# Kernel tuning notes

Hardware: AMD Instinct MI355X
Metric: run time of the kernel (lower is better)

## Reference

```python
import jax, jax.numpy as jnp
import numpy as np

B, S, D, H = 2, 2048, 1024, 16
HD = D // H
SCALING = HD ** -0.5


def _length_mask(lengths, seqlen):
    return (jnp.arange(seqlen)[None, :] < jnp.asarray(lengths)[:, None]).astype(jnp.int32)


def setup_inputs() -> dict:
    key = jax.random.key(0)
    ks = jax.random.split(key, 10)
    std = D ** -0.5
    inp = {
        "hidden_states": jax.random.normal(ks[0], (B, S, D), dtype=jnp.float32),
        "Wq": jax.random.normal(ks[1], (D, D), dtype=jnp.float32) * std,
        "bq": jax.random.normal(ks[2], (D,), dtype=jnp.float32) * 0.02,
        "Wk": jax.random.normal(ks[3], (D, D), dtype=jnp.float32) * std,
        "bk": jax.random.normal(ks[4], (D,), dtype=jnp.float32) * 0.02,
        "Wv": jax.random.normal(ks[5], (D, D), dtype=jnp.float32) * std,
        "bv": jax.random.normal(ks[6], (D,), dtype=jnp.float32) * 0.02,
        "Wo": jax.random.normal(ks[7], (D, D), dtype=jnp.float32) * std,
        "bo": jax.random.normal(ks[8], (D,), dtype=jnp.float32) * 0.02,
        # variable valid lengths per batch element (padding at the end)
        "query_mask_1d": _length_mask([S, S - 512], S),
        "key_mask_1d": _length_mask([S, S - 512], S),
    }
    return inp


def reference(hidden_states, Wq, bq, Wk, bk, Wv, bv, Wo, bo, query_mask_1d, key_mask_1d):
    bsz, tgt_len, _ = hidden_states.shape
    # projections (dropout p=0 / eval -> identity)
    q = (hidden_states @ Wq + bq) * SCALING
    k = hidden_states @ Wk + bk
    v = hidden_states @ Wv + bv
    q = q.reshape(bsz, tgt_len, H, HD).transpose(0, 2, 1, 3)  # [B,H,S,HD]
    k = k.reshape(bsz, -1, H, HD).transpose(0, 2, 1, 3)
    v = v.reshape(bsz, -1, H, HD).transpose(0, 2, 1, 3)

    scores = jnp.einsum("bhqd,bhkd->bhqk", q, k)  # [B,H,S,S]
    q_valid = (query_mask_1d != 0)[:, None, :, None]  # [B,1,S,1]
    k_valid = (key_mask_1d != 0)[:, None, None, :]    # [B,1,1,S]
    # masked_fill(-inf) on padded keys; padded-query rows would be all -inf ->
    # softmax NaN -> nan_to_num(0). We compute the same result NaN-free by
    # zeroing the scores of padded-query rows and zeroing their probs after.
    s = jnp.where(k_valid, scores, -jnp.inf)
    s = jnp.where(q_valid, s, 0.0)
    attn_weights = jax.nn.softmax(s, axis=-1) * q_valid  # == softmax + nan_to_num

    attn_output = jnp.einsum("bhqk,bhkd->bhqd", attn_weights, v)
    attn_output = attn_output.transpose(0, 2, 1, 3).reshape(bsz, tgt_len, D)
    attn_output = attn_output @ Wo + bo
    return attn_output
```

## Files before the change

### kernel.cpp

```cpp
#include <hip/hip_runtime.h>
#include <stdint.h>

#define BB 2
#define SS 2048
#define DD 1024
#define HH 16
#define HDIM 64
#define MTOT (BB*SS)
#define QK_SCALE_LOG2E 0.180336880f

typedef unsigned short u16;
typedef __attribute__((ext_vector_type(8))) __bf16 bf16x8;
typedef __attribute__((ext_vector_type(4))) float f32x4;

static __device__ __forceinline__ float exp2_hw(float x) {
    return __builtin_amdgcn_exp2f(x);
}

static __device__ __forceinline__ u16 f2bu(float f) {
    union { float f; uint32_t u; } c; c.f = f;
    uint32_t u = c.u + 0x7fffu + ((c.u >> 16) & 1u);
    return (u16)(u >> 16);
}

static __device__ __forceinline__ u16 f2b_hw(float f) {
    __bf16 b = (__bf16)f;
    union { __bf16 b; u16 u; } c; c.b = b;
    return c.u;
}

static __device__ __forceinline__ uint32_t cvt_pk_bf16(float lo, float hi) {
    uint32_t r;
    asm("v_cvt_pk_bf16_f32 %0, %1, %2" : "=v"(r) : "v"(lo), "v"(hi));
    return r;
}

static __device__ __forceinline__ void gload_lds16(const void* g, void* l) {
    __builtin_amdgcn_global_load_lds(
        (const __attribute__((address_space(1))) uint32_t*)(g),
        (__attribute__((address_space(3))) uint32_t*)(l),
        16, 0, 0);
}

__global__ void k_convert_x(const float* __restrict__ x, u16* __restrict__ xb) {
    int i = (blockIdx.x * blockDim.x + threadIdx.x) * 4;
    float4 v = *(const float4*)(x + i);
    ushort4 o;
    o.x = f2bu(v.x); o.y = f2bu(v.y); o.z = f2bu(v.z); o.w = f2bu(v.w);
    *(ushort4*)(xb + i) = o;
}

__global__ void k_transpose_w(const float* __restrict__ Wq, const float* __restrict__ Wk,
                              const float* __restrict__ Wv, const float* __restrict__ Wo,
                              u16* __restrict__ Wqkv_t, u16* __restrict__ Wo_t) {
    __shared__ float tile[32][33];
    const int which = blockIdx.z;
    const float* W = (which == 0) ? Wq : (which == 1) ? Wk : (which == 2) ? Wv : Wo;
    u16* dst = (which < 3) ? (Wqkv_t + (size_t)which * DD * DD) : Wo_t;
    const int n0 = blockIdx.x * 32, k0 = blockIdx.y * 32;
    const int tx = threadIdx.x, ty = threadIdx.y;
    #pragma unroll
    for (int i = 0; i < 32; i += 8)
        tile[ty + i][tx] = W[(size_t)(k0 + ty + i) * DD + (n0 + tx)];
    __syncthreads();
    #pragma unroll
    for (int i = 0; i < 32; i += 8)
        dst[(size_t)(n0 + ty + i) * DD + (k0 + tx)] = f2bu(tile[tx][ty + i]);
}

#define PH_BODY(BUF, Q, READB, STAGECODE, TAILWAIT)                           \
  { bf16x8 afr[2][2];                                                         \
    _Pragma("unroll") for (int m2 = 0; m2 < 2; ++m2)                          \
      _Pragma("unroll") for (int ks = 0; ks < 2; ++ks)                        \
        afr[m2][ks] = rdA(BUF, 2*(Q)+m2, ks);                                 \
    if (READB) {                                                              \
      _Pragma("unroll") for (int nf = 0; nf < 4; ++nf)                        \
        _Pragma("unroll") for (int ks = 0; ks < 2; ++ks)                      \
          bfr[nf][ks] = rdB(BUF, nf, ks);                                     \
    }                                                                         \
    STAGECODE;                                                                \
    __builtin_amdgcn_s_barrier();                                             \
    asm volatile("s_waitcnt lgkmcnt(0)" ::: "memory");                        \
    __builtin_amdgcn_sched_barrier(0);                                        \
    __builtin_amdgcn_s_setprio(1);                                            \
    _Pragma("unroll") for (int m2 = 0; m2 < 2; ++m2)                          \
      _Pragma("unroll") for (int nf = 0; nf < 4; ++nf)                        \
        _Pragma("unroll") for (int ks = 0; ks < 2; ++ks)                      \
          acc[2*(Q)+m2][nf] = __builtin_amdgcn_mfma_f32_16x16x32_bf16(        \
              afr[m2][ks], bfr[nf][ks], acc[2*(Q)+m2][nf], 0, 0, 0);          \
    __builtin_amdgcn_s_setprio(0);                                            \
    TAILWAIT;                                                                 \
    __builtin_amdgcn_s_barrier();                                             \
  }

__global__ __launch_bounds__(512, 2) void k_gemm_qkv(
    const u16* __restrict__ Xb, const u16* __restrict__ Wt,
    const float* __restrict__ bq, const float* __restrict__ bk_, const float* __restrict__ bv,
    u16* __restrict__ Qb, u16* __restrict__ Kb, u16* __restrict__ Vt)
{
    __shared__ u16 As[2][256 * 64];
    __shared__ u16 Bs[2][256 * 64];

    const int flat = blockIdx.y * 12 + blockIdx.x;
    const int swz = (flat & 7) * 24 + (flat >> 3);
    const int bx = swz % 12, by = swz / 12;
    const int m0 = by << 8, n0 = bx << 8;

    const int t = threadIdx.x;
    const int lane = t & 63, w = t >> 6;
    const int wm = (w >> 2) << 7, wn = (w & 3) << 6;
    const int lr = lane & 15, lg = lane >> 4;

    const u16* Asrc = Xb + (size_t)m0 * DD;
    const u16* Bsrc = Wt + (size_t)n0 * DD;

    f32x4 acc[8][4] = {};
    bf16x8 bfr[4][2];

    auto stgA = [&](int buf, int half, int tt) {
        #pragma unroll
        for (int r = 0; r < 2; ++r) {
            int off = (t + (r << 9)) << 4;
            int row = off >> 7, colb = off & 127;
            int scol = colb ^ ((row & 7) << 4);
            gload_lds16(Asrc + (size_t)((half << 7) + row) * DD + (tt << 6) + (scol >> 1),
                        (char*)As[buf] + (half << 14) + off);
        }
    };
    auto stgB = [&](int buf, int half, int tt) {
        #pragma unroll
        for (int r = 0; r < 2; ++r) {
            int off = (t + (r << 9)) << 4;
            int row = off >> 7, colb = off & 127;
            int scol = colb ^ ((row & 7) << 4);
            gload_lds16(Bsrc + (size_t)((half << 7) + row) * DD + (tt << 6) + (scol >> 1),
                        (char*)Bs[buf] + (half << 14) + off);
        }
    };

    auto rdA = [&](int buf, int mf, int ks) {
        const int row = wm + (mf << 4) + lr;
        const int col = ((ks << 6) + (lg << 4)) ^ ((row & 7) << 4);
        return *(const bf16x8*)((const char*)As[buf] + row * 128 + col);
    };
    auto rdB = [&](int buf, int nf, int ks) {
        const int row = wn + (nf << 4) + lr;
        const int col = ((ks << 6) + (lg << 4)) ^ ((row & 7) << 4);
        return *(const bf16x8*)((const char*)Bs[buf] + row * 128 + col);
    };

    stgA(0, 0, 0); stgA(0, 1, 0); stgB(0, 0, 0); stgB(0, 1, 0);
    stgB(1, 0, 1); stgB(1, 1, 1);
    asm volatile("s_waitcnt vmcnt(4)" ::: "memory");
    __builtin_amdgcn_s_barrier();

    #pragma unroll 1
    for (int i = 0; i < 7; ++i) {
        const int t1 = 2 * i + 1, t2 = 2 * i + 2, t3 = 2 * i + 3;
        PH_BODY(0, 0, true,  { stgA(1, 0, t1); }, {});
        PH_BODY(0, 1, false, { stgA(1, 1, t1); }, {});
        PH_BODY(0, 2, false, { stgB(0, 0, t2); }, {});
        PH_BODY(0, 3, false, { stgB(0, 1, t2); },
                { asm volatile("s_waitcnt vmcnt(4)" ::: "memory"); });
        PH_BODY(1, 0, true,  { stgA(0, 0, t2); }, {});
        PH_BODY(1, 1, false, { stgA(0, 1, t2); }, {});
        PH_BODY(1, 2, false, { stgB(1, 0, t3); }, {});
        PH_BODY(1, 3, false, { stgB(1, 1, t3); },
                { asm volatile("s_waitcnt vmcnt(4)" ::: "memory"); });
    }
    PH_BODY(0, 0, true,  { stgA(1, 0, 15); }, {});
    PH_BODY(0, 1, false, { stgA(1, 1, 15); }, {});
    PH_BODY(0, 2, false, {}, {});
    PH_BODY(0, 3, false, {},
            { asm volatile("s_waitcnt vmcnt(0)" ::: "memory"); });
    PH_BODY(1, 0, true,  {}, {});
    PH_BODY(1, 1, false, {}, {});
    PH_BODY(1, 2, false, {}, {});
    PH_BODY(1, 3, false, {}, {});

    const int which = n0 >> 10;
    #pragma unroll
    for (int mf = 0; mf < 8; ++mf) {
        #pragma unroll
        for (int nf = 0; nf < 4; ++nf) {
            const int n = n0 + wn + (nf << 4) + lr;
            const int mbase = m0 + wm + (mf << 4) + (lg << 2);
            const int b_ = mbase >> 11;
            const int s_ = mbase & 2047;
            const int nn = n & 1023;
            const int hh = nn >> 6, d = nn & 63;
            if (which == 0) {
                const float bias = bq[nn];
                u16* dstp = Qb + (((size_t)b_ * HH + hh) * SS + s_) * HDIM + d;
                #pragma unroll
                for (int r = 0; r < 4; ++r)
                    dstp[(size_t)r * HDIM] = f2bu((acc[mf][nf][r] + bias) * QK_SCALE_LOG2E);
            } else if (which == 1) {
                const float bias = bk_[nn];
                u16* dstp = Kb + (((size_t)b_ * HH + hh) * SS + s_) * HDIM + d;
                #pragma unroll
                for (int r = 0; r < 4; ++r)
                    dstp[(size_t)r * HDIM] = f2bu(acc[mf][nf][r] + bias);
            } else {
                const float bias = bv[nn];
                ushort4 pk;
                pk.x = f2bu(acc[mf][nf][0] + bias);
                pk.y = f2bu(acc[mf][nf][1] + bias);
                pk.z = f2bu(acc[mf][nf][2] + bias);
                pk.w = f2bu(acc[mf][nf][3] + bias);
                *(ushort4*)(Vt + (((size_t)b_ * HH + hh) * HDIM + d) * SS + s_) = pk;
            }
        }
    }
}

__global__ __launch_bounds__(512, 4) void k_attn(
    const u16* __restrict__ Qb, const u16* __restrict__ Kb, const u16* __restrict__ Vt,
    const int* __restrict__ qmask, const int* __restrict__ kmask,
    u16* __restrict__ X2)
{
    const int i = blockIdx.x;
    const int xcd = i & 7, j = i >> 3;
    const int qt = j & 15;
    const int bh = xcd + ((j >> 4) << 3);
    const int b_ = bh >> 4;
    const int h = bh & 15;

    const int t = threadIdx.x;
    const int lane = t & 63, w = t >> 6;
    const int lr = lane & 15, lg = lane >> 4;

    __shared__ u16 Ks[3][64 * 64];
    __shared__ u16 Vs[3][64 * 64];
    __shared__ u16 Ps[8][16 * 64];

    const int q0 = qt << 7;
    const size_t bhs = (size_t)b_ * HH + h;
    const u16* Qbase = Qb + bhs * SS * HDIM;
    const char* KbaseB = (const char*)(Kb + bhs * SS * HDIM);
    const char* VbaseB = (const char*)(Vt + bhs * HDIM * SS);

    if (qmask[b_ * SS + q0] == 0) {
        #pragma unroll
        for (int r = 0; r < 4; ++r) {
            const int q = q0 + (w << 4) + (lg << 2) + r;
            #pragma unroll
            for (int nf = 0; nf < 4; ++nf)
                X2[((size_t)b_ * SS + q) * DD + (h << 6) + (nf << 4) + lr] = 0;
        }
        return;
    }

    int kv = (lane < 32) ? kmask[b_ * SS + (lane << 6)] : 0;
    unsigned long long bal = __ballot(kv != 0);
    const int nkt = __popcll(bal);

    bf16x8 qf[2];
    #pragma unroll
    for (int ks = 0; ks < 2; ++ks)
        qf[ks] = *(const bf16x8*)(Qbase + (size_t)(q0 + (w << 4) + lr) * HDIM + (ks << 5) + (lg << 3));

    bf16x8 vones;
    #pragma unroll
    for (int i2 = 0; i2 < 8; ++i2) vones[i2] = (__bf16)1.0f;

    f32x4 o[4] = {};
    f32x4 lacc = {};

    auto stage = [&](int buf, int kb) {
        const int off = t << 4;
        const int row = off >> 7, colb = off & 127;
        const int scol = colb ^ ((row & 7) << 4);
        gload_lds16(KbaseB + (size_t)(kb + row) * 128 + scol, (char*)Ks[buf] + off);
        gload_lds16(VbaseB + ((size_t)row * SS + (size_t)kb) * 2 + scol, (char*)Vs[buf] + off);
    };

    if (nkt > 0) stage(0, 0);
    if (nkt > 1) stage(1, 64);
    if (nkt > 1) { asm volatile("s_waitcnt vmcnt(2)" ::: "memory"); }
    else         { asm volatile("s_waitcnt vmcnt(0)" ::: "memory"); }
    __builtin_amdgcn_sched_barrier(0);
    __builtin_amdgcn_s_barrier();

    u16* P = Ps[w];

    int cur = 0;
    #pragma unroll 1
    for (int kt = 0; kt < nkt; ++kt) {
        const int kb = kt << 6;
        const int nxt = (cur == 2) ? 0 : cur + 1;
        const int nx2 = (nxt == 2) ? 0 : nxt + 1;
        if (kt + 2 < nkt) stage(nx2, kb + 128);

        f32x4 sf[4] = {};
        __builtin_amdgcn_s_setprio(1);
        #pragma unroll
        for (int ks = 0; ks < 2; ++ks) {
            #pragma unroll
            for (int f = 0; f < 4; ++f) {
                const int krow = (f << 4) + lr;
                const int kcol = ((ks << 6) + (lg << 4)) ^ ((krow & 7) << 4);
                bf16x8 kf = *(const bf16x8*)((const char*)Ks[cur] + krow * 128 + kcol);
                sf[f] = __builtin_amdgcn_mfma_f32_16x16x32_bf16(kf, qf[ks], sf[f], 0, 0, 0);
            }
        }
        __builtin_amdgcn_s_setprio(0);
        if (kt == nkt - 1) {
            #pragma unroll
            for (int f = 0; f < 4; ++f) {
                #pragma unroll
                for (int r = 0; r < 4; ++r) {
                    if (kmask[b_ * SS + kb + (f << 4) + (lg << 2) + r] == 0)
                        sf[f][r] = -1e30f;
                }
            }
        }
        #pragma unroll
        for (int f = 0; f < 4; ++f)
            #pragma unroll
            for (int r = 0; r < 4; ++r)
                sf[f][r] = exp2_hw(sf[f][r]);

        #pragma unroll
        for (int f = 0; f < 4; ++f) {
            uint2 pk;
            pk.x = cvt_pk_bf16(sf[f][0], sf[f][1]);
            pk.y = cvt_pk_bf16(sf[f][2], sf[f][3]);
            *(uint2*)((char*)P + (((lr << 7) + (f << 5) + (lg << 3)) ^ ((lr & 7) << 4))) = pk;
        }

        __builtin_amdgcn_s_setprio(1);
        #pragma unroll
        for (int ks = 0; ks < 2; ++ks) {
            bf16x8 pa = *(const bf16x8*)((const char*)P + (((lr << 7) + (ks << 6) + (lg << 4)) ^ ((lr & 7) << 4)));
            lacc = __builtin_amdgcn_mfma_f32_16x16x32_bf16(pa, vones, lacc, 0, 0, 0);
            #pragma unroll
            for (int nf = 0; nf < 4; ++nf) {
                const int vrow = (nf << 4) + lr;
                const int vcol = ((ks << 6) + (lg << 4)) ^ ((vrow & 7) << 4);
                bf16x8 vb = *(const bf16x8*)((const char*)Vs[cur] + vrow * 128 + vcol);
                o[nf] = __builtin_amdgcn_mfma_f32_16x16x32_bf16(pa, vb, o[nf], 0, 0, 0);
            }
        }
        __builtin_amdgcn_s_setprio(0);

        if (kt + 2 < nkt) { asm volatile("s_waitcnt vmcnt(2)" ::: "memory"); }
        else              { asm volatile("s_waitcnt vmcnt(0)" ::: "memory"); }
        __builtin_amdgcn_sched_barrier(0);
        __builtin_amdgcn_s_barrier();
        cur = nxt;
    }

    #pragma unroll
    for (int r = 0; r < 4; ++r) {
        const int q = q0 + (w << 4) + (lg << 2) + r;
        float l = lacc[r];
        float inv = (l > 0.f) ? __builtin_amdgcn_rcpf(l) : 0.f;
        if (qmask[b_ * SS + q] == 0) inv = 0.f;
        #pragma unroll
        for (int nf = 0; nf < 4; ++nf)
            X2[((size_t)b_ * SS + q) * DD + (h << 6) + (nf << 4) + lr] = f2b_hw(o[nf][r] * inv);
    }
}

__global__ __launch_bounds__(256) void k_gemm_out(
    const u16* __restrict__ X2, const u16* __restrict__ Wot,
    const float* __restrict__ bo, float* __restrict__ out)
{
    __shared__ u16 As2[2][128 * 64];
    __shared__ u16 Bs2[2][128 * 64];
    const int m0 = blockIdx.y * 128, n0 = blockIdx.x * 128;
    const int t = threadIdx.x;
    const int lane = t & 63, w = t >> 6;
    const int wm = (w >> 1) << 6, wn = (w & 1) << 6;
    const int lr = lane & 15, lg = lane >> 4;

    f32x4 acc[4][4] = {};

    auto stage = [&](int buf, int k0) {
        #pragma unroll
        for (int i = 0; i < 4; ++i) {
            int off = (t + (i << 8)) << 4;
            int row = off >> 7, colb = off & 127;
            int scol = colb ^ ((row & 7) << 4);
            gload_lds16(X2 + (size_t)(m0 + row) * DD + k0 + (scol >> 1), (char*)As2[buf] + off);
            gload_lds16(Wot + (size_t)(n0 + row) * DD + k0 + (scol >> 1), (char*)Bs2[buf] + off);
        }
    };

    stage(0, 0);
    __syncthreads();

    int cur = 0;
    for (int kt = 0; kt < 16; ++kt) {
        if (kt < 15) stage(cur ^ 1, (kt + 1) << 6);
        #pragma unroll
        for (int ks = 0; ks < 2; ++ks) {
            bf16x8 a[4], b[4];
            #pragma unroll
            for (int i = 0; i < 4; ++i) {
                const int row = wm + (i << 4) + lr;
                a[i] = *(const bf16x8*)((const char*)As2[cur] + row * 128 + (((ks << 6) + (lg << 4)) ^ ((row & 7) << 4)));
            }
            #pragma unroll
            for (int i = 0; i < 4; ++i) {
                const int row = wn + (i << 4) + lr;
                b[i] = *(const bf16x8*)((const char*)Bs2[cur] + row * 128 + (((ks << 6) + (lg << 4)) ^ ((row & 7) << 4)));
            }
            #pragma unroll
            for (int mi = 0; mi < 4; ++mi)
                #pragma unroll
                for (int ni = 0; ni < 4; ++ni)
                    acc[mi][ni] = __builtin_amdgcn_mfma_f32_16x16x32_bf16(a[mi], b[ni], acc[mi][ni], 0, 0, 0);
        }
        __syncthreads();
        cur ^= 1;
    }

    #pragma unroll
    for (int mi = 0; mi < 4; ++mi) {
        #pragma unroll
        for (int ni = 0; ni < 4; ++ni) {
            const int n = n0 + wn + (ni << 4) + lr;
            const int mbase = m0 + wm + (mi << 4) + (lg << 2);
            const float bias = bo[n];
            #pragma unroll
            for (int r = 0; r < 4; ++r)
                out[(size_t)(mbase + r) * DD + n] = acc[mi][ni][r] + bias;
        }
    }
}

extern "C" void kernel_launch(void* const* d_in, const int* in_sizes, int n_in,
                              void* d_out, int out_size, void* d_ws, size_t ws_size,
                              hipStream_t stream) {
    const float* hs = (const float*)d_in[0];
    const float* Wq = (const float*)d_in[1];
    const float* bq = (const float*)d_in[2];
    const float* Wk = (const float*)d_in[3];
    const float* bk = (const float*)d_in[4];
    const float* Wv = (const float*)d_in[5];
    const float* bv = (const float*)d_in[6];
    const float* Wo = (const float*)d_in[7];
    const float* bo = (const float*)d_in[8];
    const int* qm = (const int*)d_in[9];
    const int* km = (const int*)d_in[10];
    float* out = (float*)d_out;

    char* ws = (char*)d_ws;
    const size_t MB = 1024 * 1024;
    u16* Xb  = (u16*)(ws + 0);
    u16* Wt3 = (u16*)(ws + 8 * MB);
    u16* Wot = (u16*)(ws + 14 * MB);
    u16* Qb  = (u16*)(ws + 16 * MB);
    u16* Kb  = (u16*)(ws + 24 * MB);
    u16* Vt  = (u16*)(ws + 32 * MB);
    u16* X2  = (u16*)(ws + 40 * MB);

    k_convert_x<<<dim3(MTOT * DD / 1024), dim3(256), 0, stream>>>(hs, Xb);
    k_transpose_w<<<dim3(32, 32, 4), dim3(32, 8), 0, stream>>>(Wq, Wk, Wv, Wo, Wt3, Wot);
    k_gemm_qkv<<<dim3(12, 16), dim3(512), 0, stream>>>(Xb, Wt3, bq, bk, bv, Qb, Kb, Vt);
    k_attn<<<dim3(512), dim3(512), 0, stream>>>(Qb, Kb, Vt, qm, km, X2);
    k_gemm_out<<<dim3(8, 32), dim3(256), 0, stream>>>(X2, Wot, bo, out);
}
```

Baseline: 117.0 us.

## Retile QKV GEMM to 256x192 tiles with triple-buffered A and XCD-aware mapping

The QKV projection GEMM tile changes from 256x256 to 256x192, so the grid grows from 192 to 256 blocks. That count maps evenly onto the 256 CUs and should reduce tail imbalance. The A operand becomes triple-buffered in LDS through rotating pointers, B stays double-buffered, and prefetch runs two K-steps ahead with a deeper vmcnt wait. Block-to-tile mapping is reworked so each XCD covers a contiguous 4x8 region for L2 reuse. In exchange, per-block arithmetic intensity is lower, LDS use is higher, and the rotated pointer and prefetch schedule is more complex, which risks errors.

```diff
diff --git a/kernel.cpp b/kernel.cpp
--- a/kernel.cpp
+++ b/kernel.cpp
@@ -68,15 +68,15 @@
         dst[(size_t)(n0 + ty + i) * DD + (k0 + tx)] = f2bu(tile[tx][ty + i]);
 }
 
-#define PH_BODY(BUF, Q, READB, STAGECODE, TAILWAIT)                           \
+#define PH(AP, Q, READB, STAGECODE, TAILWAIT)                                 \
   { bf16x8 afr[2][2];                                                         \
     _Pragma("unroll") for (int m2 = 0; m2 < 2; ++m2)                          \
       _Pragma("unroll") for (int ks = 0; ks < 2; ++ks)                        \
-        afr[m2][ks] = rdA(BUF, 2*(Q)+m2, ks);                                 \
+        afr[m2][ks] = rdA(AP, 2*(Q)+m2, ks);                                  \
     if (READB) {                                                              \
-      _Pragma("unroll") for (int nf = 0; nf < 4; ++nf)                        \
+      _Pragma("unroll") for (int nf = 0; nf < 3; ++nf)                        \
         _Pragma("unroll") for (int ks = 0; ks < 2; ++ks)                      \
-          bfr[nf][ks] = rdB(BUF, nf, ks);                                     \
+          bfr[nf][ks] = rdB(BP_, nf, ks);                                     \
     }                                                                         \
     STAGECODE;                                                                \
     __builtin_amdgcn_s_barrier();                                             \
@@ -84,7 +84,7 @@
     __builtin_amdgcn_sched_barrier(0);                                        \
     __builtin_amdgcn_s_setprio(1);                                            \
     _Pragma("unroll") for (int m2 = 0; m2 < 2; ++m2)                          \
-      _Pragma("unroll") for (int nf = 0; nf < 4; ++nf)                        \
+      _Pragma("unroll") for (int nf = 0; nf < 3; ++nf)                        \
         _Pragma("unroll") for (int ks = 0; ks < 2; ++ks)                      \
           acc[2*(Q)+m2][nf] = __builtin_amdgcn_mfma_f32_16x16x32_bf16(        \
               afr[m2][ks], bfr[nf][ks], acc[2*(Q)+m2][nf], 0, 0, 0);          \
@@ -93,109 +93,127 @@
     __builtin_amdgcn_s_barrier();                                             \
   }
 
+#define QITER(AE, AO, AS2, TB)                                                \
+  { const u16* BP_ = Bs0;                                                     \
+    PH(AE, 0, true,  { stgA(AS2, 0, (TB)+2); }, {});                          \
+    PH(AE, 1, false, { stgA(AS2, 1, (TB)+2); }, {});                          \
+    PH(AE, 2, false, { stgB(Bs0, (TB)+2); }, {});                             \
+    PH(AE, 3, false, {},                                                      \
+       { asm volatile("s_waitcnt vmcnt(7)" ::: "memory"); }); }               \
+  { const u16* BP_ = Bs1;                                                     \
+    PH(AO, 0, true,  { stgA(AE, 0, (TB)+3); }, {});                           \
+    PH(AO, 1, false, { stgA(AE, 1, (TB)+3); }, {});                           \
+    PH(AO, 2, false, { stgB(Bs1, (TB)+3); }, {});                             \
+    PH(AO, 3, false, {},                                                      \
+       { asm volatile("s_waitcnt vmcnt(7)" ::: "memory"); }); }
+
+#define QITERP(AE, AO)                                                        \
+  { const u16* BP_ = Bs0;                                                     \
+    PH(AE, 0, true,  {}, {});                                                 \
+    PH(AE, 1, false, {}, {});                                                 \
+    PH(AE, 2, false, {}, {});                                                 \
+    PH(AE, 3, false, {},                                                      \
+       { asm volatile("s_waitcnt vmcnt(0)" ::: "memory"); }); }               \
+  { const u16* BP_ = Bs1;                                                     \
+    PH(AO, 0, true,  {}, {});                                                 \
+    PH(AO, 1, false, {}, {});                                                 \
+    PH(AO, 2, false, {}, {});                                                 \
+    PH(AO, 3, false, {}, {}); }
+
 __global__ __launch_bounds__(512, 2) void k_gemm_qkv(
     const u16* __restrict__ Xb, const u16* __restrict__ Wt,
     const float* __restrict__ bq, const float* __restrict__ bk_, const float* __restrict__ bv,
     u16* __restrict__ Qb, u16* __restrict__ Kb, u16* __restrict__ Vt)
 {
-    __shared__ u16 As[2][256 * 64];
-    __shared__ u16 Bs[2][256 * 64];
-
-    const int flat = blockIdx.y * 12 + blockIdx.x;
-    const int swz = (flat & 7) * 24 + (flat >> 3);
-    const int bx = swz % 12, by = swz / 12;
-    const int m0 = by << 8, n0 = bx << 8;
+    __shared__ u16 AsA[3][256 * 64];
+    __shared__ u16 BsB[2][192 * 64];
+
+    const int flat = blockIdx.y * 16 + blockIdx.x;
+    const int xcd = flat & 7, idx = flat >> 3;
+    const int by = ((xcd >> 1) << 2) + (idx >> 3);
+    const int bx = ((xcd & 1) << 3) + (idx & 7);
+    const int m0 = by << 8, n0 = bx * 192;
 
     const int t = threadIdx.x;
     const int lane = t & 63, w = t >> 6;
-    const int wm = (w >> 2) << 7, wn = (w & 3) << 6;
+    const int wm = (w >> 2) << 7, wn = (w & 3) * 48;
     const int lr = lane & 15, lg = lane >> 4;
 
     const u16* Asrc = Xb + (size_t)m0 * DD;
     const u16* Bsrc = Wt + (size_t)n0 * DD;
 
-    f32x4 acc[8][4] = {};
-    bf16x8 bfr[4][2];
-
-    auto stgA = [&](int buf, int half, int tt) {
+    f32x4 acc[8][3] = {};
+    bf16x8 bfr[3][2];
+
+    auto stgA = [&](u16* bufp, int half, int tt) {
         #pragma unroll
         for (int r = 0; r < 2; ++r) {
             int off = (t + (r << 9)) << 4;
             int row = off >> 7, colb = off & 127;
             int scol = colb ^ ((row & 7) << 4);
             gload_lds16(Asrc + (size_t)((half << 7) + row) * DD + (tt << 6) + (scol >> 1),
-                        (char*)As[buf] + (half << 14) + off);
-        }
-    };
-    auto stgB = [&](int buf, int half, int tt) {
-        #pragma unroll
-        for (int r = 0; r < 2; ++r) {
+                        (char*)bufp + (half << 14) + off);
+        }
+    };
+    auto stgB = [&](u16* bufp, int tt) {
+        #pragma unroll
+        for (int r = 0; r < 3; ++r) {
             int off = (t + (r << 9)) << 4;
             int row = off >> 7, colb = off & 127;
             int scol = colb ^ ((row & 7) << 4);
-            gload_lds16(Bsrc + (size_t)((half << 7) + row) * DD + (tt << 6) + (scol >> 1),
-                        (char*)Bs[buf] + (half << 14) + off);
-        }
-    };
-
-    auto rdA = [&](int buf, int mf, int ks) {
+            gload_lds16(Bsrc + (size_t)row * DD + (tt << 6) + (scol >> 1),
+                        (char*)bufp + off);
+        }
+    };
+
+    auto rdA = [&](const u16* bufp, int mf, int ks) {
         const int row = wm + (mf << 4) + lr;
         const int col = ((ks << 6) + (lg << 4)) ^ ((row & 7) << 4);
-        return *(const bf16x8*)((const char*)As[buf] + row * 128 + col);
-    };
-    auto rdB = [&](int buf, int nf, int ks) {
+        return *(const bf16x8*)((const char*)bufp + row * 128 + col);
+    };
+    auto rdB = [&](const u16* bufp, int nf, int ks) {
         const int row = wn + (nf << 4) + lr;
         const int col = ((ks << 6) + (lg << 4)) ^ ((row & 7) << 4);
-        return *(const bf16x8*)((const char*)Bs[buf] + row * 128 + col);
-    };
-
-    stgA(0, 0, 0); stgA(0, 1, 0); stgB(0, 0, 0); stgB(0, 1, 0);
-    stgB(1, 0, 1); stgB(1, 1, 1);
-    asm volatile("s_waitcnt vmcnt(4)" ::: "memory");
+        return *(const bf16x8*)((const char*)bufp + row * 128 + col);
+    };
+
+    u16* pA0 = AsA[0]; u16* pA1 = AsA[1]; u16* pA2 = AsA[2];
+    u16* Bs0 = BsB[0]; u16* Bs1 = BsB[1];
+
+    stgA(pA0, 0, 0); stgA(pA0, 1, 0); stgB(Bs0, 0);
+    stgA(pA1, 0, 1); stgA(pA1, 1, 1); stgB(Bs1, 1);
+    asm volatile("s_waitcnt vmcnt(7)" ::: "memory");
+    __builtin_amdgcn_sched_barrier(0);
     __builtin_amdgcn_s_barrier();
 
     #pragma unroll 1
-    for (int i = 0; i < 7; ++i) {
-        const int t1 = 2 * i + 1, t2 = 2 * i + 2, t3 = 2 * i + 3;
-        PH_BODY(0, 0, true,  { stgA(1, 0, t1); }, {});
-        PH_BODY(0, 1, false, { stgA(1, 1, t1); }, {});
-        PH_BODY(0, 2, false, { stgB(0, 0, t2); }, {});
-        PH_BODY(0, 3, false, { stgB(0, 1, t2); },
-                { asm volatile("s_waitcnt vmcnt(4)" ::: "memory"); });
-        PH_BODY(1, 0, true,  { stgA(0, 0, t2); }, {});
-        PH_BODY(1, 1, false, { stgA(0, 1, t2); }, {});
-        PH_BODY(1, 2, false, { stgB(1, 0, t3); }, {});
-        PH_BODY(1, 3, false, { stgB(1, 1, t3); },
-                { asm volatile("s_waitcnt vmcnt(4)" ::: "memory"); });
-    }
-    PH_BODY(0, 0, true,  { stgA(1, 0, 15); }, {});
-    PH_BODY(0, 1, false, { stgA(1, 1, 15); }, {});
-    PH_BODY(0, 2, false, {}, {});
-    PH_BODY(0, 3, false, {},
-            { asm volatile("s_waitcnt vmcnt(0)" ::: "memory"); });
-    PH_BODY(1, 0, true,  {}, {});
-    PH_BODY(1, 1, false, {}, {});
-    PH_BODY(1, 2, false, {}, {});
-    PH_BODY(1, 3, false, {}, {});
-
-    const int which = n0 >> 10;
+    for (int j = 0; j < 2; ++j) {
+        const int tb = j * 6;
+        QITER(pA0, pA1, pA2, tb);
+        QITER(pA2, pA0, pA1, tb + 2);
+        QITER(pA1, pA2, pA0, tb + 4);
+    }
+    QITER(pA0, pA1, pA2, 12);
+    QITERP(pA2, pA0);
+
     #pragma unroll
     for (int mf = 0; mf < 8; ++mf) {
         #pragma unroll
-        for (int nf = 0; nf < 4; ++nf) {
+        for (int nf = 0; nf < 3; ++nf) {
             const int n = n0 + wn + (nf << 4) + lr;
             const int mbase = m0 + wm + (mf << 4) + (lg << 2);
             const int b_ = mbase >> 11;
             const int s_ = mbase & 2047;
+            const int seg = n >> 10;
             const int nn = n & 1023;
             const int hh = nn >> 6, d = nn & 63;
-            if (which == 0) {
+            if (seg == 0) {
                 const float bias = bq[nn];
                 u16* dstp = Qb + (((size_t)b_ * HH + hh) * SS + s_) * HDIM + d;
                 #pragma unroll
                 for (int r = 0; r < 4; ++r)
                     dstp[(size_t)r * HDIM] = f2bu((acc[mf][nf][r] + bias) * QK_SCALE_LOG2E);
-            } else if (which == 1) {
+            } else if (seg == 1) {
                 const float bias = bk_[nn];
                 u16* dstp = Kb + (((size_t)b_ * HH + hh) * SS + s_) * HDIM + d;
                 #pragma unroll
@@ -459,7 +477,7 @@
 
     k_convert_x<<<dim3(MTOT * DD / 1024), dim3(256), 0, stream>>>(hs, Xb);
     k_transpose_w<<<dim3(32, 32, 4), dim3(32, 8), 0, stream>>>(Wq, Wk, Wv, Wo, Wt3, Wot);
-    k_gemm_qkv<<<dim3(12, 16), dim3(512), 0, stream>>>(Xb, Wt3, bq, bk, bv, Qb, Kb, Vt);
+    k_gemm_qkv<<<dim3(16, 16), dim3(512), 0, stream>>>(Xb, Wt3, bq, bk, bv, Qb, Kb, Vt);
     k_attn<<<dim3(512), dim3(512), 0, stream>>>(Qb, Kb, Vt, qm, km, X2);
     k_gemm_out<<<dim3(8, 32), dim3(256), 0, stream>>>(X2, Wot, bo, out);
 }
```

Measured after the change: 113.0 us. 3.5% less time.
